# Optimization experiments

Measured on AMD Instinct MI355X. Metric: run time of the kernel, lower is better.

## Reference

```python
import jax, jax.numpy as jnp
import numpy as np

D = 768      # hidden_size
L = 4        # num_hidden_layers
H = 12       # num_attention_heads
I = 3072     # intermediate_size
B, S = 2, 2048
EPS = 1e-5


def setup_inputs() -> dict:
    key = jax.random.key(0)
    ks = jax.random.split(key, 8)
    sc = 0.02
    return {
        "x": jax.random.normal(ks[0], (B, S, D), dtype=jnp.float32),
        # weights stored as [in, out] so y = x @ W + b (same math as torch Linear)
        "qkv_w": jax.random.normal(ks[1], (L, D, 3 * D), dtype=jnp.float32) * sc,
        "qkv_b": jnp.zeros((L, 3 * D), dtype=jnp.float32),
        "out_w": jax.random.normal(ks[2], (L, D, D), dtype=jnp.float32) * sc,
        "out_b": jnp.zeros((L, D), dtype=jnp.float32),
        "ln1_w": jnp.ones((L, D), dtype=jnp.float32),
        "ln1_b": jnp.zeros((L, D), dtype=jnp.float32),
        "fc1_w": jax.random.normal(ks[3], (L, D, I), dtype=jnp.float32) * sc,
        "fc1_b": jnp.zeros((L, I), dtype=jnp.float32),
        "fc2_w": jax.random.normal(ks[4], (L, I, D), dtype=jnp.float32) * sc,
        "fc2_b": jnp.zeros((L, D), dtype=jnp.float32),
        "ln2_w": jnp.ones((L, D), dtype=jnp.float32),
        "ln2_b": jnp.zeros((L, D), dtype=jnp.float32),
    }


def _layer_norm(x, w, b):
    mu = jnp.mean(x, axis=-1, keepdims=True)
    var = jnp.mean(jnp.square(x - mu), axis=-1, keepdims=True)
    return (x - mu) * jax.lax.rsqrt(var + EPS) * w + b


def _encoder(x, qkv_w, qkv_b, out_w, out_b, ln1_w, ln1_b,
             fc1_w, fc1_b, fc2_w, fc2_b, ln2_w, ln2_b):
    hd = D // H
    scale = 1.0 / jnp.sqrt(jnp.float32(hd))

    def block(x, p):
        (qw, qb, ow, ob, l1w, l1b, f1w, f1b, f2w, f2b, l2w, l2b) = p
        # --- attention sub-block (pre-norm residual) ---
        h = _layer_norm(x, l1w, l1b)
        qkv = h @ qw + qb                      # [B,S,3D]
        qkv = qkv.reshape(B, S, H, 3 * hd).transpose(0, 2, 1, 3)  # [B,H,S,3hd]
        q, k, v = jnp.split(qkv, 3, axis=-1)
        logits = jnp.einsum('bhqd,bhkd->bhqk', q, k) * scale       # [B,H,S,S]
        attn = jax.nn.softmax(logits, axis=-1)
        vals = jnp.einsum('bhqk,bhkd->bhqd', attn, v)              # [B,H,S,hd]
        vals = vals.transpose(0, 2, 1, 3).reshape(B, S, D)
        x = x + vals @ ow + ob
        # --- MLP sub-block (pre-norm residual) ---
        h = _layer_norm(x, l2w, l2b)
        h = jax.nn.gelu(h @ f1w + f1b, approximate=False)
        x = x + h @ f2w + f2b
        return x, None

    params = (qkv_w, qkv_b, out_w, out_b, ln1_w, ln1_b,
              fc1_w, fc1_b, fc2_w, fc2_b, ln2_w, ln2_b)
    x, _ = jax.lax.scan(block, x, params)
    return x


def reference(x, qkv_w, qkv_b, out_w, out_b, ln1_w, ln1_b,
              fc1_w, fc1_b, fc2_w, fc2_b, ln2_w, ln2_b):
    return _encoder(x, qkv_w, qkv_b, out_w, out_b, ln1_w, ln1_b,
                    fc1_w, fc1_b, fc2_w, fc2_b, ln2_w, ln2_b)
```

## Files before the change

### kernel.cpp

```cpp
#include <hip/hip_runtime.h>
#include <stdint.h>
#include <math.h>

#define D_MODEL 768
#define NTOK    4096
#define SEQ     2048
#define NHEAD   12
#define HDIM    64
#define D_FF    3072
#define QKV_N   2304

typedef unsigned short ushort_t;
typedef short  short8 __attribute__((ext_vector_type(8)));
typedef float  f32x4  __attribute__((ext_vector_type(4)));
typedef float  f32x16 __attribute__((ext_vector_type(16)));

__device__ __forceinline__ float b2f(ushort_t u) {
  union { unsigned int u; float f; } v; v.u = ((unsigned int)u) << 16; return v.f;
}
__device__ __forceinline__ ushort_t f2b(float f) {
  union { float f; unsigned int u; } v; v.f = f;
  unsigned int u = v.u;
  return (ushort_t)((u + 0x7fffu + ((u >> 16) & 1u)) >> 16);
}
__device__ __forceinline__ unsigned cvtpk_bf16(float lo, float hi) {
  unsigned r;
  asm("v_cvt_pk_bf16_f32 %0, %1, %2" : "=v"(r) : "v"(lo), "v"(hi));
  return r;
}

__global__ __launch_bounds__(256) void transpose_layers(
    const float* __restrict__ qkv_w, const float* __restrict__ out_w,
    const float* __restrict__ fc1_w, const float* __restrict__ fc2_w,
    ushort_t* __restrict__ qkvT, ushort_t* __restrict__ outT,
    ushort_t* __restrict__ f1T, ushort_t* __restrict__ f2T) {
  __shared__ ushort_t tile[32][33];
  int bid = blockIdx.x;
  size_t l = blockIdx.y;
  const float* src; ushort_t* dst; int K, N, tn, tk;
  if (bid < 1728)      { src = qkv_w + l * D_MODEL * QKV_N; dst = qkvT + l * D_MODEL * QKV_N;
                         K = 768;  N = 2304; tn = bid % 72;  tk = bid / 72; }
  else if (bid < 2304) { int b = bid - 1728; src = out_w + l * D_MODEL * D_MODEL; dst = outT + l * D_MODEL * D_MODEL;
                         K = 768;  N = 768;  tn = b % 24; tk = b / 24; }
  else if (bid < 4608) { int b = bid - 2304; src = fc1_w + l * D_MODEL * D_FF; dst = f1T + l * D_MODEL * D_FF;
                         K = 768;  N = 3072; tn = b % 96; tk = b / 96; }
  else                 { int b = bid - 4608; src = fc2_w + l * D_FF * D_MODEL; dst = f2T + l * D_FF * D_MODEL;
                         K = 3072; N = 768;  tn = b % 24; tk = b / 24; }
  int n0 = tn * 32, k0 = tk * 32;
  int tx = threadIdx.x, ty = threadIdx.y;
  #pragma unroll
  for (int i = 0; i < 32; i += 8)
    tile[ty + i][tx] = f2b(src[(size_t)(k0 + ty + i) * N + n0 + tx]);
  __syncthreads();
  #pragma unroll
  for (int i = 0; i < 32; i += 8)
    dst[(size_t)(n0 + ty + i) * K + k0 + tx] = tile[tx][ty + i];
}

__global__ __launch_bounds__(256) void ln_kernel(const float* __restrict__ x,
                                                 const float* __restrict__ w,
                                                 const float* __restrict__ b,
                                                 ushort_t* __restrict__ out) {
  __shared__ float red[4];
  int tok = blockIdx.x, t = threadIdx.x;
  const float* xr = x + (size_t)tok * D_MODEL;
  float v0 = xr[t], v1 = xr[t + 256], v2 = xr[t + 512];
  float s = v0 + v1 + v2;
  #pragma unroll
  for (int o = 1; o < 64; o <<= 1) s += __shfl_xor(s, o, 64);
  if ((t & 63) == 0) red[t >> 6] = s;
  __syncthreads();
  float mean = (red[0] + red[1] + red[2] + red[3]) * (1.0f / 768.0f);
  __syncthreads();
  float d0 = v0 - mean, d1 = v1 - mean, d2 = v2 - mean;
  float q = d0 * d0 + d1 * d1 + d2 * d2;
  #pragma unroll
  for (int o = 1; o < 64; o <<= 1) q += __shfl_xor(q, o, 64);
  if ((t & 63) == 0) red[t >> 6] = q;
  __syncthreads();
  float var = (red[0] + red[1] + red[2] + red[3]) * (1.0f / 768.0f);
  float rs = rsqrtf(var + 1e-5f);
  ushort_t* orow = out + (size_t)tok * D_MODEL;
  orow[t]       = f2b(d0 * rs * w[t]       + b[t]);
  orow[t + 256] = f2b(d1 * rs * w[t + 256] + b[t + 256]);
  orow[t + 512] = f2b(d2 * rs * w[t + 512] + b[t + 512]);
}

template <int EPI, int TN>
__global__ __launch_bounds__(256) void gemm_kernel(
    const ushort_t* __restrict__ A, const ushort_t* __restrict__ BT,
    const float* __restrict__ bias,
    ushort_t* __restrict__ Cb, int M, int N, int K) {
  constexpr int NI = 4;
  __shared__ ushort_t As[2][128 * 32];
  __shared__ ushort_t Bs[2][TN * 32];
  int t = threadIdx.x;
  int lane = t & 63, wave = t >> 6;
  int gx = gridDim.x;
  int nwg = gx * gridDim.y;
  int bid0 = blockIdx.y * gx + blockIdx.x;
  int qn = nwg >> 3, rm = nwg & 7;
  int xcd = bid0 & 7, pos = bid0 >> 3;
  int wg = (xcd < rm ? xcd * (qn + 1) : rm * (qn + 1) + (xcd - rm) * qn) + pos;
  int m0 = (wg / gx) * 128, n0 = (wg % gx) * TN;
  int wm = (wave & 1) * 64;
  int wn = (wave >> 1) * 64;
  int quad = lane >> 4, l16 = lane & 15;
  int kq = quad * 8;
  int lrow = lane >> 2, lcol = (lane & 3) * 8;

  auto stage = [&](int k0, int buf) {
    #pragma unroll
    for (int c = 0; c < 2; ++c) {
      int rowA = wave * 32 + c * 16 + lrow;
      const ushort_t* ga = A + (size_t)(m0 + rowA) * K + k0 + lcol;
      ushort_t* la = &As[buf][(wave * 32 + c * 16) * 32];
      __builtin_amdgcn_global_load_lds((const __attribute__((address_space(1))) void*)ga,
                                       (__attribute__((address_space(3))) void*)la, 16, 0, 0);
      const ushort_t* gb = BT + (size_t)(n0 + rowA) * K + k0 + lcol;
      ushort_t* lb = &Bs[buf][(wave * 32 + c * 16) * 32];
      __builtin_amdgcn_global_load_lds((const __attribute__((address_space(1))) void*)gb,
                                       (__attribute__((address_space(3))) void*)lb, 16, 0, 0);
    }
  };

  f32x4 acc[NI][4];
  #pragma unroll
  for (int i = 0; i < NI; ++i)
    #pragma unroll
    for (int j = 0; j < 4; ++j) acc[i][j] = (f32x4){0.f, 0.f, 0.f, 0.f};

  stage(0, 0);
  int nk = K / 32;
  for (int ki = 0; ki < nk; ++ki) {
    int cur = ki & 1;
    __syncthreads();
    if (ki + 1 < nk) stage((ki + 1) * 32, cur ^ 1);
    short8 af[NI], bf[4];
    #pragma unroll
    for (int i = 0; i < NI; ++i)
      af[i] = *(const short8*)&As[cur][(wm + i * 16 + l16) * 32 + kq];
    #pragma unroll
    for (int j = 0; j < 4; ++j)
      bf[j] = *(const short8*)&Bs[cur][(wn + j * 16 + l16) * 32 + kq];
    #pragma unroll
    for (int i = 0; i < NI; ++i)
      #pragma unroll
      for (int j = 0; j < 4; ++j)
        acc[i][j] = __builtin_amdgcn_mfma_f32_16x16x32_bf16(af[i], bf[j], acc[i][j], 0, 0, 0);
  }

  #pragma unroll
  for (int i = 0; i < NI; ++i) {
    #pragma unroll
    for (int j = 0; j < 4; ++j) {
      int col = n0 + wn + j * 16 + l16;
      float bv = bias[col];
      #pragma unroll
      for (int r = 0; r < 4; ++r) {
        int row = m0 + wm + i * 16 + quad * 4 + r;
        float v = acc[i][j][r] + bv;
        if (EPI == 1) {
          float u = v + 0.044715f * v * v * v;
          u = fminf(u, 30.0f);
          float e = exp2f(2.302207848f * u);
          v = v * e / (e + 1.0f);
        }
        Cb[(size_t)row * N + col] = f2b(v);
      }
    }
  }
}

__global__ __launch_bounds__(256) void gemm64_kernel(
    const ushort_t* __restrict__ A, const ushort_t* __restrict__ BT,
    const float* __restrict__ bias, const float* __restrict__ resid,
    float* __restrict__ Cf, int M, int N, int K) {
  __shared__ ushort_t As[2][64 * 32];
  __shared__ ushort_t Bs[2][64 * 32];
  int t = threadIdx.x;
  int lane = t & 63, wave = t >> 6;
  int gx = gridDim.x;
  int nwg = gx * gridDim.y;
  int bid0 = blockIdx.y * gx + blockIdx.x;
  int qn = nwg >> 3, rm = nwg & 7;
  int xcd = bid0 & 7, pos = bid0 >> 3;
  int wg = (xcd < rm ? xcd * (qn + 1) : rm * (qn + 1) + (xcd - rm) * qn) + pos;
  int m0 = (wg / gx) * 64, n0 = (wg % gx) * 64;
  int wm = (wave & 1) * 32, wn = (wave >> 1) * 32;
  int quad = lane >> 4, l16 = lane & 15;
  int kq = quad * 8;
  int lrow = lane >> 2, lcol = (lane & 3) * 8;

  auto stage = [&](int k0, int buf) {
    int row = wave * 16 + lrow;
    const ushort_t* ga = A + (size_t)(m0 + row) * K + k0 + lcol;
    ushort_t* la = &As[buf][(wave * 16) * 32];
    __builtin_amdgcn_global_load_lds((const __attribute__((address_space(1))) void*)ga,
                                     (__attribute__((address_space(3))) void*)la, 16, 0, 0);
    const ushort_t* gb = BT + (size_t)(n0 + row) * K + k0 + lcol;
    ushort_t* lb = &Bs[buf][(wave * 16) * 32];
    __builtin_amdgcn_global_load_lds((const __attribute__((address_space(1))) void*)gb,
                                     (__attribute__((address_space(3))) void*)lb, 16, 0, 0);
  };

  f32x4 acc[2][2];
  #pragma unroll
  for (int i = 0; i < 2; ++i)
    #pragma unroll
    for (int j = 0; j < 2; ++j) acc[i][j] = (f32x4){0.f, 0.f, 0.f, 0.f};

  stage(0, 0);
  int nk = K / 32;
  for (int ki = 0; ki < nk; ++ki) {
    int cur = ki & 1;
    __syncthreads();
    if (ki + 1 < nk) stage((ki + 1) * 32, cur ^ 1);
    short8 af[2], bf[2];
    #pragma unroll
    for (int i = 0; i < 2; ++i)
      af[i] = *(const short8*)&As[cur][(wm + i * 16 + l16) * 32 + kq];
    #pragma unroll
    for (int j = 0; j < 2; ++j)
      bf[j] = *(const short8*)&Bs[cur][(wn + j * 16 + l16) * 32 + kq];
    #pragma unroll
    for (int i = 0; i < 2; ++i)
      #pragma unroll
      for (int j = 0; j < 2; ++j)
        acc[i][j] = __builtin_amdgcn_mfma_f32_16x16x32_bf16(af[i], bf[j], acc[i][j], 0, 0, 0);
  }

  #pragma unroll
  for (int i = 0; i < 2; ++i) {
    #pragma unroll
    for (int j = 0; j < 2; ++j) {
      int col = n0 + wn + j * 16 + l16;
      float bv = bias[col];
      #pragma unroll
      for (int r = 0; r < 4; ++r) {
        int row = m0 + wm + i * 16 + quad * 4 + r;
        float v = acc[i][j][r] + bv + resid[(size_t)row * N + col];
        Cf[(size_t)row * N + col] = v;
      }
    }
  }
}

__global__ __launch_bounds__(256, 3) void attn_kernel(const ushort_t* __restrict__ qkv,
                                                      ushort_t* __restrict__ out) {
  __shared__ __align__(16) ushort_t Ks[2][64 * 72];
  __shared__ __align__(16) ushort_t Vt[2][64 * 72];
  int t = threadIdx.x;
  int lane = t & 63, wave = t >> 6;
  int l31 = lane & 31, h = lane >> 5, h8 = h * 8;
  int kh = wave & 1, qh = wave >> 1;
  int kw = kh * 32;
  int qt = blockIdx.x;
  int bh = blockIdx.y;
  int b = bh / NHEAD, hd = bh % NHEAD;
  size_t base = (size_t)b * SEQ * QKV_N + hd * 192;

  const float kscale = 0.125f * 1.44269504088896f;

  short8 qf[4];
  {
    const ushort_t* qp = qkv + base + (size_t)(qt * 64 + qh * 32 + l31) * QKV_N + h8;
    #pragma unroll
    for (int ks = 0; ks < 4; ++ks) qf[ks] = *(const short8*)(qp + ks * 16);
  }

  int krow = t >> 1, kcol = (t & 1) * 32;
  int kcb = krow >> 6, krl = krow & 63;
  int kp = t & 63, vdb = (t >> 6) * 16;
  int vcb = kp >> 5, kpl = kp & 31;
  short8 kr[4], va[2], vb[2];
  auto kv_load = [&](int sbase) {
    const ushort_t* gk = qkv + base + (size_t)(sbase + krow) * QKV_N + 64 + kcol;
    #pragma unroll
    for (int i = 0; i < 4; ++i) kr[i] = *(const short8*)(gk + i * 8);
    const ushort_t* gv = qkv + base + (size_t)(sbase + 2 * kp) * QKV_N + 128 + vdb;
    va[0] = *(const short8*)gv;           va[1] = *(const short8*)(gv + 8);
    vb[0] = *(const short8*)(gv + QKV_N); vb[1] = *(const short8*)(gv + QKV_N + 8);
  };
  auto kv_write = [&]() {
    #pragma unroll
    for (int i = 0; i < 4; ++i)
      *(short8*)&Ks[kcb][krl * 72 + kcol + i * 8] = kr[i];
    unsigned* vtw = (unsigned*)&Vt[vcb][0];
    #pragma unroll
    for (int half = 0; half < 2; ++half)
      #pragma unroll
      for (int e = 0; e < 8; ++e) {
        unsigned pk = (unsigned)(unsigned short)va[half][e] |
                      ((unsigned)(unsigned short)vb[half][e] << 16);
        vtw[(vdb + half * 8 + e) * 36 + kpl] = pk;
      }
  };

  f32x16 o0, o1;
  #pragma unroll
  for (int i = 0; i < 16; ++i) { o0[i] = 0.f; o1[i] = 0.f; }
  float ls = 0.f;

  kv_load(0);
  for (int it = 0; it < SEQ / 128; ++it) {
    kv_write();
    __syncthreads();
    if (it + 1 < SEQ / 128) kv_load((it + 1) * 128);

    #pragma unroll
    for (int c = 0; c < 2; ++c) {
      f32x16 s;
      #pragma unroll
      for (int i = 0; i < 16; ++i) s[i] = 0.f;
      __builtin_amdgcn_s_setprio(1);
      #pragma unroll
      for (int ks = 0; ks < 4; ++ks) {
        short8 kf = *(const short8*)&Ks[c][(kw + l31) * 72 + ks * 16 + h8];
        s = __builtin_amdgcn_mfma_f32_32x32x16_bf16(kf, qf[ks], s, 0, 0, 0);
      }
      __builtin_amdgcn_s_setprio(0);

      unsigned wpk[4][2];
      #pragma unroll
      for (int g = 0; g < 4; ++g) {
        float p0 = exp2f(s[4 * g + 0] * kscale), p1 = exp2f(s[4 * g + 1] * kscale);
        float p2 = exp2f(s[4 * g + 2] * kscale), p3 = exp2f(s[4 * g + 3] * kscale);
        ls += (p0 + p1) + (p2 + p3);
        wpk[g][0] = cvtpk_bf16(p0, p1);
        wpk[g][1] = cvtpk_bf16(p2, p3);
      }

      #pragma unroll
      for (int k4 = 0; k4 < 2; ++k4) {
        int j2 = k4 * 2;
        unsigned f[4];
        #pragma unroll
        for (int c2 = 0; c2 < 2; ++c2) {
          unsigned a  = wpk[j2][c2];
          unsigned b2 = wpk[j2 + 1][c2];
          unsigned snd = h ? a : b2;
          unsigned rcv = (unsigned)__shfl_xor((int)snd, 32, 64);
          f[c2]     = h ? rcv : a;
          f[2 + c2] = h ? b2 : rcv;
        }
        union { unsigned u[4]; short8 s8; } uc;
        uc.u[0] = f[0]; uc.u[1] = f[1]; uc.u[2] = f[2]; uc.u[3] = f[3];
        short8 ap = uc.s8;
        short8 v0 = *(const short8*)&Vt[c][(l31)      * 72 + kw + k4 * 16 + h8];
        short8 v1 = *(const short8*)&Vt[c][(32 + l31) * 72 + kw + k4 * 16 + h8];
        __builtin_amdgcn_s_setprio(1);
        o0 = __builtin_amdgcn_mfma_f32_32x32x16_bf16(ap, v0, o0, 0, 0, 0);
        o1 = __builtin_amdgcn_mfma_f32_32x32x16_bf16(ap, v1, o1, 0, 0, 0);
        __builtin_amdgcn_s_setprio(0);
      }
    }
    __syncthreads();
  }

  float* slab = (float*)&Ks[0][0];
  if (kh == 1) {
    float* s = slab + (size_t)(qh * 64 + lane) * 33;
    #pragma unroll
    for (int i = 0; i < 16; ++i) { s[i] = o0[i]; s[16 + i] = o1[i]; }
    s[32] = ls;
  }
  __syncthreads();
  if (kh == 0) {
    float* s = slab + (size_t)(qh * 64 + lane) * 33;
    #pragma unroll
    for (int i = 0; i < 16; ++i) { o0[i] += s[i]; o1[i] += s[16 + i]; }
    ls += s[32];
    ls += __shfl_xor(ls, 32, 64);

    size_t ob = (size_t)(b * SEQ + qt * 64 + qh * 32) * D_MODEL + hd * HDIM;
    #pragma unroll
    for (int g = 0; g < 4; ++g) {
      #pragma unroll
      for (int r = 0; r < 4; ++r) {
        int reg = 4 * g + r;
        int qrow = 8 * g + 4 * h + r;
        float inv = 1.0f / __shfl(ls, qrow, 64);
        ushort_t* orow = out + ob + (size_t)qrow * D_MODEL;
        orow[l31]      = f2b(o0[reg] * inv);
        orow[32 + l31] = f2b(o1[reg] * inv);
      }
    }
  }
}

extern "C" void kernel_launch(void* const* d_in, const int* in_sizes, int n_in,
                              void* d_out, int out_size, void* d_ws, size_t ws_size,
                              hipStream_t stream) {
  const float* x_in  = (const float*)d_in[0];
  const float* qkv_w = (const float*)d_in[1];
  const float* qkv_b = (const float*)d_in[2];
  const float* out_w = (const float*)d_in[3];
  const float* out_b = (const float*)d_in[4];
  const float* ln1_w = (const float*)d_in[5];
  const float* ln1_b = (const float*)d_in[6];
  const float* fc1_w = (const float*)d_in[7];
  const float* fc1_b = (const float*)d_in[8];
  const float* fc2_w = (const float*)d_in[9];
  const float* fc2_b = (const float*)d_in[10];
  const float* ln2_w = (const float*)d_in[11];
  const float* ln2_b = (const float*)d_in[12];

  char* ws = (char*)d_ws;
  size_t off = 0;
  auto alloc = [&](size_t bytes) -> void* {
    void* p = ws + off; off += (bytes + 255) & ~(size_t)255; return p;
  };
  float*    buf_x  = (float*)   alloc((size_t)NTOK * D_MODEL * 4);
  float*    buf_x2 = (float*)   alloc((size_t)NTOK * D_MODEL * 4);
  ushort_t* bigb   = (ushort_t*)alloc((size_t)NTOK * D_FF * 2);
  ushort_t* h_b    = (ushort_t*)alloc((size_t)NTOK * D_MODEL * 2);
  ushort_t* at_b   = (ushort_t*)alloc((size_t)NTOK * D_MODEL * 2);

  size_t per_layer_w = ((size_t)QKV_N * D_MODEL + (size_t)D_MODEL * D_MODEL +
                        (size_t)D_FF * D_MODEL * 2) * 2;
  bool all_layers = (ws_size >= off + 4 * per_layer_w + (4 << 10));
  int nl = all_layers ? 4 : 1;
  ushort_t* qkvT = (ushort_t*)alloc((size_t)QKV_N * D_MODEL * 2 * nl);
  ushort_t* outT = (ushort_t*)alloc((size_t)D_MODEL * D_MODEL * 2 * nl);
  ushort_t* f1T  = (ushort_t*)alloc((size_t)D_FF * D_MODEL * 2 * nl);
  ushort_t* f2T  = (ushort_t*)alloc((size_t)D_MODEL * D_FF * 2 * nl);

  ushort_t* qkv_a = bigb;
  ushort_t* mlp_b = bigb;

  if (all_layers)
    transpose_layers<<<dim3(6912, 4), dim3(32, 8), 0, stream>>>(
        qkv_w, out_w, fc1_w, fc2_w, qkvT, outT, f1T, f2T);

  for (int l = 0; l < 4; ++l) {
    const float* resid_in = (l == 0) ? x_in : buf_x;
    size_t lw = all_layers ? (size_t)l : 0;
    ushort_t* qkvT_l = qkvT + lw * QKV_N * D_MODEL;
    ushort_t* outT_l = outT + lw * D_MODEL * D_MODEL;
    ushort_t* f1T_l  = f1T  + lw * D_FF * D_MODEL;
    ushort_t* f2T_l  = f2T  + lw * D_MODEL * D_FF;
    if (!all_layers)
      transpose_layers<<<dim3(6912, 1), dim3(32, 8), 0, stream>>>(
          qkv_w + (size_t)l * D_MODEL * QKV_N, out_w + (size_t)l * D_MODEL * D_MODEL,
          fc1_w + (size_t)l * D_MODEL * D_FF,  fc2_w + (size_t)l * D_FF * D_MODEL,
          qkvT_l, outT_l, f1T_l, f2T_l);
    ln_kernel<<<NTOK, 256, 0, stream>>>(resid_in, ln1_w + l * D_MODEL, ln1_b + l * D_MODEL, h_b);
    gemm_kernel<0, 128><<<dim3(QKV_N / 128, NTOK / 128), 256, 0, stream>>>(
        h_b, qkvT_l, qkv_b + l * QKV_N, qkv_a, NTOK, QKV_N, D_MODEL);
    attn_kernel<<<dim3(SEQ / 64, 2 * NHEAD), 256, 0, stream>>>(qkv_a, at_b);
    gemm64_kernel<<<dim3(D_MODEL / 64, NTOK / 64), 256, 0, stream>>>(
        at_b, outT_l, out_b + l * D_MODEL, resid_in, buf_x2, NTOK, D_MODEL, D_MODEL);
    ln_kernel<<<NTOK, 256, 0, stream>>>(buf_x2, ln2_w + l * D_MODEL, ln2_b + l * D_MODEL, h_b);
    gemm_kernel<1, 128><<<dim3(D_FF / 128, NTOK / 128), 256, 0, stream>>>(
        h_b, f1T_l, fc1_b + l * D_FF, mlp_b, NTOK, D_FF, D_MODEL);
    float* x_next = (l < 3) ? buf_x : (float*)d_out;
    gemm64_kernel<<<dim3(D_MODEL / 64, NTOK / 64), 256, 0, stream>>>(
        mlp_b, f2T_l, fc2_b + l * D_MODEL, buf_x2, x_next, NTOK, D_MODEL, D_FF);
  }
  (void)in_sizes; (void)n_in; (void)out_size;
}
```

Baseline: 944.1 us.

## Split-K the FC2 GEMM and fuse partial combine with next-layer LayerNorm

Replaces the 64x64-tile FC2 GEMM (K=3072) with a 128x128-tile split-K kernel across 4 K-slices writing fp32 partials. A new combine kernel then sums the partials with bias and residual and applies the next layer's LN1, so the separate ln_kernel launch is skipped for layers 1-3. The aim is more parallelism and better tile reuse for the long-K GEMM. The cost is an extra 4x fp32 partial buffer, about 50 MB of extra write and read traffic per layer.

```diff
diff --git a/kernel.cpp b/kernel.cpp
--- a/kernel.cpp
+++ b/kernel.cpp
@@ -84,6 +84,44 @@
   orow[t]       = f2b(d0 * rs * w[t]       + b[t]);
   orow[t + 256] = f2b(d1 * rs * w[t + 256] + b[t + 256]);
   orow[t + 512] = f2b(d2 * rs * w[t + 512] + b[t + 512]);
+}
+
+template <int DO_LN>
+__global__ __launch_bounds__(256) void combine_ln_kernel(
+    const float* __restrict__ P, const float* __restrict__ bias,
+    const float* __restrict__ resid, const float* __restrict__ w,
+    const float* __restrict__ b, float* __restrict__ xout,
+    ushort_t* __restrict__ h) {
+  __shared__ float red[4];
+  int tok = blockIdx.x, t = threadIdx.x;
+  size_t ro = (size_t)tok * D_MODEL;
+  const size_t PS = (size_t)NTOK * D_MODEL;
+  int c0 = t, c1 = t + 256, c2 = t + 512;
+  float v0 = bias[c0] + resid[ro + c0] + P[ro + c0] + P[PS + ro + c0] + P[2 * PS + ro + c0] + P[3 * PS + ro + c0];
+  float v1 = bias[c1] + resid[ro + c1] + P[ro + c1] + P[PS + ro + c1] + P[2 * PS + ro + c1] + P[3 * PS + ro + c1];
+  float v2 = bias[c2] + resid[ro + c2] + P[ro + c2] + P[PS + ro + c2] + P[2 * PS + ro + c2] + P[3 * PS + ro + c2];
+  xout[ro + c0] = v0; xout[ro + c1] = v1; xout[ro + c2] = v2;
+  if constexpr (DO_LN) {
+    float s = v0 + v1 + v2;
+    #pragma unroll
+    for (int o = 1; o < 64; o <<= 1) s += __shfl_xor(s, o, 64);
+    if ((t & 63) == 0) red[t >> 6] = s;
+    __syncthreads();
+    float mean = (red[0] + red[1] + red[2] + red[3]) * (1.0f / 768.0f);
+    __syncthreads();
+    float d0 = v0 - mean, d1 = v1 - mean, d2 = v2 - mean;
+    float q = d0 * d0 + d1 * d1 + d2 * d2;
+    #pragma unroll
+    for (int o = 1; o < 64; o <<= 1) q += __shfl_xor(q, o, 64);
+    if ((t & 63) == 0) red[t >> 6] = q;
+    __syncthreads();
+    float var = (red[0] + red[1] + red[2] + red[3]) * (1.0f / 768.0f);
+    float rs = rsqrtf(var + 1e-5f);
+    ushort_t* orow = h + ro;
+    orow[c0] = f2b(d0 * rs * w[c0] + b[c0]);
+    orow[c1] = f2b(d1 * rs * w[c1] + b[c1]);
+    orow[c2] = f2b(d2 * rs * w[c2] + b[c2]);
+  }
 }
 
 template <int EPI, int TN>
@@ -172,6 +210,82 @@
   }
 }
 
+__global__ __launch_bounds__(256) void gemm_splitk_kernel(
+    const ushort_t* __restrict__ A, const ushort_t* __restrict__ BT,
+    float* __restrict__ P, int M, int N, int K, int KS) {
+  __shared__ ushort_t As[2][128 * 32];
+  __shared__ ushort_t Bs[2][128 * 32];
+  int t = threadIdx.x;
+  int lane = t & 63, wave = t >> 6;
+  int gx = gridDim.x;
+  int nwg = gx * gridDim.y;
+  int bid0 = blockIdx.y * gx + blockIdx.x;
+  int qn = nwg >> 3, rm = nwg & 7;
+  int xcd = bid0 & 7, pos = bid0 >> 3;
+  int wg = (xcd < rm ? xcd * (qn + 1) : rm * (qn + 1) + (xcd - rm) * qn) + pos;
+  int m0 = (wg / gx) * 128, n0 = (wg % gx) * 128;
+  int kbase = blockIdx.z * KS;
+  int wm = (wave & 1) * 64, wn = (wave >> 1) * 64;
+  int quad = lane >> 4, l16 = lane & 15;
+  int kq = quad * 8;
+  int lrow = lane >> 2, lcol = (lane & 3) * 8;
+
+  auto stage = [&](int k0, int buf) {
+    #pragma unroll
+    for (int c = 0; c < 2; ++c) {
+      int rowA = wave * 32 + c * 16 + lrow;
+      const ushort_t* ga = A + (size_t)(m0 + rowA) * K + kbase + k0 + lcol;
+      ushort_t* la = &As[buf][(wave * 32 + c * 16) * 32];
+      __builtin_amdgcn_global_load_lds((const __attribute__((address_space(1))) void*)ga,
+                                       (__attribute__((address_space(3))) void*)la, 16, 0, 0);
+      const ushort_t* gb = BT + (size_t)(n0 + rowA) * K + kbase + k0 + lcol;
+      ushort_t* lb = &Bs[buf][(wave * 32 + c * 16) * 32];
+      __builtin_amdgcn_global_load_lds((const __attribute__((address_space(1))) void*)gb,
+                                       (__attribute__((address_space(3))) void*)lb, 16, 0, 0);
+    }
+  };
+
+  f32x4 acc[4][4];
+  #pragma unroll
+  for (int i = 0; i < 4; ++i)
+    #pragma unroll
+    for (int j = 0; j < 4; ++j) acc[i][j] = (f32x4){0.f, 0.f, 0.f, 0.f};
+
+  stage(0, 0);
+  int nk = KS / 32;
+  for (int ki = 0; ki < nk; ++ki) {
+    int cur = ki & 1;
+    __syncthreads();
+    if (ki + 1 < nk) stage((ki + 1) * 32, cur ^ 1);
+    short8 af[4], bf[4];
+    #pragma unroll
+    for (int i = 0; i < 4; ++i)
+      af[i] = *(const short8*)&As[cur][(wm + i * 16 + l16) * 32 + kq];
+    #pragma unroll
+    for (int j = 0; j < 4; ++j)
+      bf[j] = *(const short8*)&Bs[cur][(wn + j * 16 + l16) * 32 + kq];
+    #pragma unroll
+    for (int i = 0; i < 4; ++i)
+      #pragma unroll
+      for (int j = 0; j < 4; ++j)
+        acc[i][j] = __builtin_amdgcn_mfma_f32_16x16x32_bf16(af[i], bf[j], acc[i][j], 0, 0, 0);
+  }
+
+  float* Pz = P + (size_t)blockIdx.z * M * N;
+  #pragma unroll
+  for (int i = 0; i < 4; ++i) {
+    #pragma unroll
+    for (int j = 0; j < 4; ++j) {
+      int col = n0 + wn + j * 16 + l16;
+      #pragma unroll
+      for (int r = 0; r < 4; ++r) {
+        int row = m0 + wm + i * 16 + quad * 4 + r;
+        Pz[(size_t)row * N + col] = acc[i][j][r];
+      }
+    }
+  }
+}
+
 __global__ __launch_bounds__(256) void gemm64_kernel(
     const ushort_t* __restrict__ A, const ushort_t* __restrict__ BT,
     const float* __restrict__ bias, const float* __restrict__ resid,
@@ -417,9 +531,17 @@
   ushort_t* h_b    = (ushort_t*)alloc((size_t)NTOK * D_MODEL * 2);
   ushort_t* at_b   = (ushort_t*)alloc((size_t)NTOK * D_MODEL * 2);
 
-  size_t per_layer_w = ((size_t)QKV_N * D_MODEL + (size_t)D_MODEL * D_MODEL +
-                        (size_t)D_FF * D_MODEL * 2) * 2;
-  bool all_layers = (ws_size >= off + 4 * per_layer_w + (4 << 10));
+  size_t off_base = off;
+  size_t pl_w = ((size_t)QKV_N * D_MODEL + (size_t)D_MODEL * D_MODEL +
+                 (size_t)D_FF * D_MODEL * 2) * 2;
+  size_t splitk_bytes = (size_t)4 * NTOK * D_MODEL * 4;
+  bool use_splitk, all_layers;
+  size_t slack = 64 << 10;
+  if (ws_size >= off_base + splitk_bytes + 4 * pl_w + slack)      { use_splitk = true;  all_layers = true;  }
+  else if (ws_size >= off_base + splitk_bytes + pl_w + slack)     { use_splitk = true;  all_layers = false; }
+  else if (ws_size >= off_base + 4 * pl_w + slack)                { use_splitk = false; all_layers = true;  }
+  else                                                            { use_splitk = false; all_layers = false; }
+  float* Pbuf = use_splitk ? (float*)alloc(splitk_bytes) : nullptr;
   int nl = all_layers ? 4 : 1;
   ushort_t* qkvT = (ushort_t*)alloc((size_t)QKV_N * D_MODEL * 2 * nl);
   ushort_t* outT = (ushort_t*)alloc((size_t)D_MODEL * D_MODEL * 2 * nl);
@@ -445,7 +567,8 @@
           qkv_w + (size_t)l * D_MODEL * QKV_N, out_w + (size_t)l * D_MODEL * D_MODEL,
           fc1_w + (size_t)l * D_MODEL * D_FF,  fc2_w + (size_t)l * D_FF * D_MODEL,
           qkvT_l, outT_l, f1T_l, f2T_l);
-    ln_kernel<<<NTOK, 256, 0, stream>>>(resid_in, ln1_w + l * D_MODEL, ln1_b + l * D_MODEL, h_b);
+    if (l == 0 || !use_splitk)
+      ln_kernel<<<NTOK, 256, 0, stream>>>(resid_in, ln1_w + l * D_MODEL, ln1_b + l * D_MODEL, h_b);
     gemm_kernel<0, 128><<<dim3(QKV_N / 128, NTOK / 128), 256, 0, stream>>>(
         h_b, qkvT_l, qkv_b + l * QKV_N, qkv_a, NTOK, QKV_N, D_MODEL);
     attn_kernel<<<dim3(SEQ / 64, 2 * NHEAD), 256, 0, stream>>>(qkv_a, at_b);
@@ -454,9 +577,21 @@
     ln_kernel<<<NTOK, 256, 0, stream>>>(buf_x2, ln2_w + l * D_MODEL, ln2_b + l * D_MODEL, h_b);
     gemm_kernel<1, 128><<<dim3(D_FF / 128, NTOK / 128), 256, 0, stream>>>(
         h_b, f1T_l, fc1_b + l * D_FF, mlp_b, NTOK, D_FF, D_MODEL);
-    float* x_next = (l < 3) ? buf_x : (float*)d_out;
-    gemm64_kernel<<<dim3(D_MODEL / 64, NTOK / 64), 256, 0, stream>>>(
-        mlp_b, f2T_l, fc2_b + l * D_MODEL, buf_x2, x_next, NTOK, D_MODEL, D_FF);
+    if (use_splitk) {
+      gemm_splitk_kernel<<<dim3(D_MODEL / 128, NTOK / 128, 4), 256, 0, stream>>>(
+          mlp_b, f2T_l, Pbuf, NTOK, D_MODEL, D_FF, D_FF / 4);
+      if (l < 3)
+        combine_ln_kernel<1><<<NTOK, 256, 0, stream>>>(
+            Pbuf, fc2_b + l * D_MODEL, buf_x2,
+            ln1_w + (l + 1) * D_MODEL, ln1_b + (l + 1) * D_MODEL, buf_x, h_b);
+      else
+        combine_ln_kernel<0><<<NTOK, 256, 0, stream>>>(
+            Pbuf, fc2_b + 3 * D_MODEL, buf_x2, nullptr, nullptr, (float*)d_out, nullptr);
+    } else {
+      float* x_next = (l < 3) ? buf_x : (float*)d_out;
+      gemm64_kernel<<<dim3(D_MODEL / 64, NTOK / 64), 256, 0, stream>>>(
+          mlp_b, f2T_l, fc2_b + l * D_MODEL, buf_x2, x_next, NTOK, D_MODEL, D_FF);
+    }
   }
   (void)in_sizes; (void)n_in; (void)out_size;
 }
```

Result: faster. 890.2 us, median of 2 (-5.7%).
